# Kernel optimization log

Measured on AMD Instinct MI355X. Metric: run time of the kernel, lower is better.

The kernel has to match this reference:

```python
import jax, jax.numpy as jnp
import numpy as np

EPS = 1e-5
SLOPE = 0.2  # leakyrelu negative slope (gcn_lib default)
K = 9

def knn_idx(x, k):
    # x: (B, C, N) -> idx (B, N, k) of k nearest neighbors, self excluded
    B, C, N = x.shape
    xx = jnp.sum(x * x, axis=1)                       # (B, N)
    inner = jnp.einsum('bcn,bcm->bnm', x, x)          # (B, N, N)
    dist = xx[:, :, None] - 2.0 * inner + xx[:, None, :]
    dist = dist + jnp.eye(N, dtype=x.dtype) * 1e10    # mask self
    _, idx = jax.lax.top_k(-dist, k)                  # nearest = largest -dist
    return idx

def bn(h, g, b, axes):
    m = jnp.mean(h, axis=axes, keepdims=True)
    v = jnp.var(h, axis=axes, keepdims=True)
    sh = [1] * h.ndim; sh[1] = -1
    return (h - m) / jnp.sqrt(v + EPS) * g.reshape(sh) + b.reshape(sh)

def leaky(h):
    return jnp.where(h >= 0, h, SLOPE * h)

def edge_conv(x, idx, W, g, b):
    # x: (B, C, N); idx: (B, N, k); W: (O, 2C)
    B, C, N = x.shape
    k = idx.shape[-1]
    x_j = jax.vmap(lambda xb, ib: xb[:, ib])(x, idx)  # (B, C, N, k)
    x_i = jnp.broadcast_to(x[:, :, :, None], (B, C, N, k))
    edge = jnp.concatenate([x_i, x_j - x_i], axis=1)  # (B, 2C, N, k)
    h = jnp.einsum('oc,bcnk->bonk', W, edge)
    h = leaky(bn(h, g, b, (0, 2, 3)))
    return jnp.max(h, axis=-1)                        # (B, O, N)

def setup_inputs() -> dict:
    key = jax.random.key(0)
    ks = jax.random.split(key, 24)
    B, N = 8, 4096
    d = {}
    d['x'] = jax.random.normal(ks[0], (B, 3, N), dtype=jnp.float32)
    d['coords'] = jax.random.normal(ks[1], (B, 3, N), dtype=jnp.float32)
    def w(k_, o, i): return jax.random.normal(k_, (o, i), dtype=jnp.float32) * (2.0 / i) ** 0.5
    # edge conv layers (bias=False, batchnorm affine)
    d['w1'], d['g1'], d['b1'] = w(ks[2], 64, 6),    jnp.ones(64),  jnp.zeros(64)
    d['w2'], d['g2'], d['b2'] = w(ks[3], 64, 128),  jnp.ones(64),  jnp.zeros(64)
    d['w3'], d['g3'], d['b3'] = w(ks[4], 128, 128), jnp.ones(128), jnp.zeros(128)
    d['w4'], d['g4'], d['b4'] = w(ks[5], 256, 256), jnp.ones(256), jnp.zeros(256)
    # decoder fusion conv [512 -> 1024]
    d['wf'], d['bf'] = w(ks[6], 1024, 512), jnp.zeros(1024)
    d['gf'], d['betaf'] = jnp.ones(1024), jnp.zeros(1024)
    # classifier [2048 -> 512 -> 256 -> 40]
    d['wc1'], d['bc1'] = w(ks[7], 512, 2048), jnp.zeros(512)
    d['gc1'], d['betac1'] = jnp.ones(512), jnp.zeros(512)
    d['wc2'], d['bc2'] = w(ks[8], 256, 512), jnp.zeros(256)
    d['gc2'], d['betac2'] = jnp.ones(256), jnp.zeros(256)
    d['wc3'], d['bc3'] = w(ks[9], 40, 256), jnp.zeros(40)
    return d

def reference(x, coords, w1, g1, b1, w2, g2, b2, w3, g3, b3, w4, g4, b4,
              wf, bf, gf, betaf, wc1, bc1, gc1, betac1, wc2, bc2, gc2, betac2, wc3, bc3):
    out1 = edge_conv(x,    knn_idx(x, K),    w1, g1, b1)   # (B, 64, N)
    out2 = edge_conv(out1, knn_idx(out1, K), w2, g2, b2)   # (B, 64, N)
    out3 = edge_conv(out2, knn_idx(out2, K), w3, g3, b3)   # (B, 128, N)
    out4 = edge_conv(out3, knn_idx(out3, K), w4, g4, b4)   # (B, 256, N)
    feat = jnp.concatenate([out1, out2, out3, out4], axis=1)  # (B, 512, N)
    fusion = jnp.einsum('oc,bcn->bon', wf, feat) + bf[None, :, None]
    fusion = leaky(bn(fusion, gf, betaf, (0, 2)))           # (B, 1024, N)
    x1 = jnp.max(fusion, axis=-1)                           # adaptive max pool
    x2 = jnp.mean(fusion, axis=-1)                          # adaptive avg pool
    h = jnp.concatenate([x1, x2], axis=1)                   # (B, 2048)
    h = leaky(bn(h @ wc1.T + bc1, gc1, betac1, (0,)))       # dropout = identity (eval)
    h = leaky(bn(h @ wc2.T + bc2, gc2, betac2, (0,)))
    logits = h @ wc3.T + bc3                                # (B, 40)
    return logits
```

## Files before the change

kernel.cpp:

```cpp
#include <hip/hip_runtime.h>
#include <math.h>
#include <float.h>


#define LEAKY(y) ((y) >= 0.f ? (y) : 0.2f * (y))

using f32x16 = __attribute__((ext_vector_type(16))) float;
using bf16x8 = __attribute__((ext_vector_type(8))) __bf16;
using short8v = __attribute__((ext_vector_type(8))) short;

__device__ inline ushort f2bf(float x) {
  unsigned u = __float_as_uint(x);
  unsigned r = (u + 0x7fff + ((u >> 16) & 1)) >> 16;
  return (ushort)r;
}

template<int C>
__global__ void xx_kernel(const float* __restrict__ xin, long bstride, int N,
                          float* __restrict__ xxg) {
  int n = blockIdx.x * 256 + threadIdx.x;
  int b = blockIdx.y;
  if (n < N) {
    const float* xb = xin + (long)b * bstride;
    float s = 0.f;
    #pragma unroll
    for (int c = 0; c < C; ++c) { float t = xb[(long)c * N + n]; s += t * t; }
    xxg[(long)b * N + n] = s;
  }
}

template<int C, int KCc>
__global__ __launch_bounds__(256) void pack3_kernel(const float* __restrict__ xin, long bstride,
                                                    int N, const float* __restrict__ xxg,
                                                    ushort* __restrict__ packR,
                                                    ushort* __restrict__ packC,
                                                    float* __restrict__ xpm) {
  __shared__ float xt[C][32];
  const int tid = threadIdx.x;
  const int pb = blockIdx.x, b = blockIdx.y;
  for (int i = tid; i < C * 32; i += 256) {
    int c = i >> 5, j = i & 31;
    xt[c][j] = xin[(long)b * bstride + (long)c * N + pb * 32 + j];
  }
  __syncthreads();
  for (int i = tid; i < 32 * C; i += 256) {
    int pt = i / C, c = i % C;
    xpm[((long)b * N + pb * 32 + pt) * C + c] = xt[c][pt];
  }
  const int PB = N >> 5;
  for (int it = tid; it < KCc * 64; it += 256) {
    int kc = it >> 6, l = it & 63;
    int pt = l & 31;
    union { ushort u[8]; short8v v; } R, Cc;
    #pragma unroll
    for (int e = 0; e < 8; ++e) {
      int kp = kc * 16 + ((l >> 5) << 3) + e;
      ushort rv = 0, cv = 0;
      if (kp < 3 * C) {
        int s = kp / C, c = kp % C;
        float xv = xt[c][pt];
        ushort hi = f2bf(xv);
        float hif = __uint_as_float((unsigned)hi << 16);
        ushort mid = f2bf(xv - hif);
        rv = (s == 2) ? mid : hi;
        cv = (s == 1) ? mid : hi;
      } else if (kp == 3 * C) {
        float xxv = xxg[(long)b * N + pb * 32 + pt];
        cv = f2bf(xxv);
        rv = 0xBF00;
      } else if (kp == 3 * C + 1) {
        float xxv = xxg[(long)b * N + pb * 32 + pt];
        ushort hi = f2bf(xxv);
        float hif = __uint_as_float((unsigned)hi << 16);
        cv = f2bf(xxv - hif);
        rv = 0xBF00;
      }
      R.u[e] = rv; Cc.u[e] = cv;
    }
    long off = (((long)b * PB + pb) * KCc + kc) * 512 + l * 8;
    *reinterpret_cast<short8v*>(&packR[off]) = R.v;
    *reinterpret_cast<short8v*>(&packC[off]) = Cc.v;
  }
}

#define KNN_SCAN(SELF)                                            \
  _Pragma("unroll")                                               \
  for (int reg = 0; reg < 16; ++reg) {                            \
    int m_loc = (reg & 3) + 8 * (reg >> 2) + 4 * hf;              \
    float d = fmaf(-2.0f, acc[reg], xr);                          \
    d = fmaxf(d, 0.f);                                            \
    unsigned key = (__float_as_uint(d) & KEYMASK) |               \
                   (unsigned)((t << 5) | m_loc);                  \
    if (SELF && ((mb << 5) | m_loc) == n_glob) key = 0xFFFFFFFFu; \
    if (key < tk[9]) {                                            \
      unsigned kc = key;                                          \
      _Pragma("unroll")                                           \
      for (int s_ = 0; s_ < 10; ++s_) {                           \
        unsigned mn_ = min(kc, tk[s_]);                           \
        kc = max(kc, tk[s_]);                                     \
        tk[s_] = mn_;                                             \
      }                                                           \
    }                                                             \
  }

template<int KCc, int MINW, int Z>
__global__ __launch_bounds__(256, MINW) void knn_v5(const ushort* __restrict__ packR,
                                                    const ushort* __restrict__ packC,
                                                    const float* __restrict__ xxg,
                                                    int N, int* __restrict__ cand) {
  constexpr int SA_ELEMS = KCc * 512;
  constexpr int SA_BYTES = SA_ELEMS * 2;
  constexpr int POOL = (2 * SA_BYTES > 10240) ? 2 * SA_BYTES : 10240;
  __shared__ __align__(16) char smem[POOL];
  ushort* const sA0 = (ushort*)smem;
  ushort* const sA1 = (ushort*)(smem + SA_BYTES);

  const int tid = threadIdx.x;
  const int b = blockIdx.y, rowblk = blockIdx.x, z = blockIdx.z;
  const int w = tid >> 6, l = tid & 63;
  const int lane31 = l & 31, hf = l >> 5;
  const int PB = N >> 5;
  const int HALF = PB / Z;
  const unsigned IDXMASK = (unsigned)(HALF * 32 - 1);
  const unsigned KEYMASK = ~IDXMASK;
  const int myblk = rowblk * 4 + w;

  const ushort* rp = packR + (((long)b * PB + myblk) * (long)KCc) * 512 + l * 8;
  bf16x8 bfr[KCc];
  #pragma unroll
  for (int kc = 0; kc < KCc; ++kc)
    bfr[kc] = *reinterpret_cast<const bf16x8*>(rp + kc * 512);

  const ushort* srcb = packC + ((long)b * PB) * (long)SA_ELEMS;
  const int mb0 = z * HALF;

  {
    const ushort* src = srcb + (long)mb0 * SA_ELEMS;
    for (int i = tid * 8; i < SA_ELEMS; i += 2048)
      __builtin_amdgcn_global_load_lds(
          (const __attribute__((address_space(1))) void*)(src + i),
          (__attribute__((address_space(3))) void*)(sA0 + i), 16, 0, 0);
  }

  const int n_glob = rowblk * 128 + w * 32 + lane31;
  const float xr = xxg[(long)b * N + n_glob];

  unsigned tk[10];
  #pragma unroll
  for (int s = 0; s < 10; ++s) tk[s] = 0xFFFFFFFFu;

  __syncthreads();

  for (int t = 0; t < HALF; ++t) {
    const int mb = mb0 + t;
    const ushort* curA = (t & 1) ? sA1 : sA0;
    ushort* nxtA = (t & 1) ? sA0 : sA1;
    if (t + 1 < HALF) {
      const ushort* src = srcb + (long)(mb + 1) * SA_ELEMS;
      for (int i = tid * 8; i < SA_ELEMS; i += 2048)
        __builtin_amdgcn_global_load_lds(
            (const __attribute__((address_space(1))) void*)(src + i),
            (__attribute__((address_space(3))) void*)(nxtA + i), 16, 0, 0);
    }
    f32x16 acc = {};
    #pragma unroll
    for (int kc = 0; kc < KCc; ++kc) {
      bf16x8 af = *reinterpret_cast<const bf16x8*>(curA + kc * 512 + l * 8);
      acc = __builtin_amdgcn_mfma_f32_32x32x16_bf16(af, bfr[kc], acc, 0, 0, 0);
    }
    if (mb == myblk) {
      KNN_SCAN(true)
    } else {
      KNN_SCAN(false)
    }
    __syncthreads();
  }

  unsigned* mK = (unsigned*)smem;
  const int row = w * 32 + lane31;
  #pragma unroll
  for (int s = 0; s < 10; ++s)
    mK[row * 20 + hf * 10 + s] = tk[s];
  __syncthreads();
  if (tid < 128) {
    int p0 = 0, p1 = 0;
    const long ob = ((long)b * N + rowblk * 128 + tid) * (Z * 10) + z * 10;
    const int base_m = z * HALF * 32;
    for (int s = 0; s < 10; ++s) {
      unsigned k0 = mK[tid * 20 + p0];
      unsigned k1 = mK[tid * 20 + 10 + p1];
      bool t0 = k0 < k1;
      unsigned kk = t0 ? k0 : k1;
      cand[ob + s] = base_m + (int)(kk & IDXMASK);
      if (t0) ++p0; else ++p1;
    }
  }
}

template<int C, int P>
__global__ __launch_bounds__(320) void rerank_kernel(const float* __restrict__ xpm,
                                                     int N, const float* __restrict__ xxg,
                                                     const int* __restrict__ cand,
                                                     int* __restrict__ idx_out) {
  constexpr int ROWS = 320 / P;
  __shared__ float sq[ROWS][C];
  __shared__ float sd[ROWS][P + 1];
  __shared__ int   si[ROWS][P + 1];
  const int tid = threadIdx.x;
  const int b = blockIdx.y, n0 = blockIdx.x * ROWS;
  const float* xb = xpm + (long)b * N * C;
  for (int i = tid; i < ROWS * C; i += 320) {
    int r = i / C, c = i % C;
    sq[r][c] = xb[(long)(n0 + r) * C + c];
  }
  __syncthreads();
  const int r = tid / P, j = tid % P;
  const int n = n0 + r;
  const int m = cand[((long)b * N + n) * P + j];
  const float* cv = xb + (long)m * C;
  float dot = 0.f;
  if constexpr ((C & 3) == 0) {
    for (int c = 0; c < C; c += 4) {
      float4 v4 = *reinterpret_cast<const float4*>(cv + c);
      dot = fmaf(sq[r][c + 0], v4.x, dot);
      dot = fmaf(sq[r][c + 1], v4.y, dot);
      dot = fmaf(sq[r][c + 2], v4.z, dot);
      dot = fmaf(sq[r][c + 3], v4.w, dot);
    }
  } else {
    for (int c = 0; c < C; ++c) dot = fmaf(sq[r][c], cv[c], dot);
  }
  float d = (xxg[(long)b * N + n] - 2.0f * dot) + xxg[(long)b * N + m];
  if (m == n) d = 3.0e38f;
  sd[r][j] = d; si[r][j] = m;
  __syncthreads();
  int rank = 0;
  #pragma unroll
  for (int t = 0; t < P; ++t) {
    float dd = sd[r][t]; int ii = si[r][t];
    if (dd < d || (dd == d && ii < m)) rank++;
  }
  if (rank < 9) idx_out[((long)b * N + n) * 9 + rank] = m;
}

template<int C, int KCX>
__global__ __launch_bounds__(256) void pack6_x(const float* __restrict__ xin, long bstride,
                                               int N, ushort* __restrict__ packX) {
  __shared__ float xt[C][32];
  const int tid = threadIdx.x;
  const int pb = blockIdx.x, b = blockIdx.y;
  for (int i = tid; i < C * 32; i += 256) {
    int c = i >> 5, j = i & 31;
    xt[c][j] = xin[(long)b * bstride + (long)c * N + pb * 32 + j];
  }
  __syncthreads();
  const int PB = N >> 5;
  for (int it = tid; it < KCX * 64; it += 256) {
    int kc = it >> 6, l = it & 63;
    int pt = l & 31;
    union { ushort u[8]; short8v v; } P;
    #pragma unroll
    for (int e = 0; e < 8; ++e) {
      int kp = kc * 16 + ((l >> 5) << 3) + e;
      ushort val = 0;
      if (kp < 6 * C) {
        int s = kp / C, c = kp % C;
        float xv = xt[c][pt];
        ushort hi = f2bf(xv);
        float hif = __uint_as_float((unsigned)hi << 16);
        float r1 = xv - hif;
        ushort mid = f2bf(r1);
        float midf = __uint_as_float((unsigned)mid << 16);
        ushort lo = f2bf(r1 - midf);
        val = (s == 1 || s == 3) ? mid : ((s == 4) ? lo : hi);
      }
      P.u[e] = val;
    }
    long off = (((long)b * PB + pb) * KCX + kc) * 512 + l * 8;
    *reinterpret_cast<short8v*>(&packX[off]) = P.v;
  }
}

template<int C, int NOB, int KCW>
__global__ __launch_bounds__(256) void pack6_w(const float* __restrict__ W,
                                               ushort* __restrict__ packAw) {
  __shared__ float wt[32][C + 1];
  const int mo = blockIdx.x;
  const int mat = mo / NOB, ob = mo % NOB;
  const int tid = threadIdx.x;
  for (int i = tid; i < 32 * C; i += 256) {
    int o = i / C, c = i % C;
    float w1v = W[(long)(ob * 32 + o) * 2 * C + c];
    float w2v = W[(long)(ob * 32 + o) * 2 * C + C + c];
    wt[o][c] = mat ? w2v : (w1v - w2v);
  }
  __syncthreads();
  for (int it = tid; it < KCW * 64; it += 256) {
    int kc = it >> 6, l = it & 63;
    union { ushort u[8]; short8v v; } P;
    #pragma unroll
    for (int e = 0; e < 8; ++e) {
      int kp = kc * 16 + ((l >> 5) << 3) + e;
      ushort val = 0;
      if (kp < 6 * C) {
        int s = kp / C, c = kp % C;
        float xv = wt[l & 31][c];
        ushort hi = f2bf(xv);
        float hif = __uint_as_float((unsigned)hi << 16);
        float r1 = xv - hif;
        ushort mid = f2bf(r1);
        float midf = __uint_as_float((unsigned)mid << 16);
        ushort lo = f2bf(r1 - midf);
        val = (s == 2 || s == 3) ? mid : ((s == 5) ? lo : hi);
      }
      P.u[e] = val;
    }
    *reinterpret_cast<short8v*>(&packAw[((long)mo * KCW + kc) * 512 + l * 8]) = P.v;
  }
}

template<int KCW, int NOB>
__global__ __launch_bounds__(256) void edge_gemm6(const ushort* __restrict__ packX,
                                                  const ushort* __restrict__ packAw,
                                                  int N,
                                                  float* __restrict__ u,
                                                  float* __restrict__ v) {
  constexpr int NT = 2 * NOB;
  constexpr int TPW = NT / 4;
  constexpr int O = NOB * 32;
  const int nb = blockIdx.x, b = blockIdx.y;
  const int w = threadIdx.x >> 6, l = threadIdx.x & 63;
  const int lane31 = l & 31, hf = l >> 5;
  const ushort* xp = packX + ((long)(b * (N >> 5) + nb) * KCW) * 512 + l * 8;

  f32x16 acc[TPW] = {};
  const ushort* aptr[TPW];
  #pragma unroll
  for (int ti = 0; ti < TPW; ++ti) {
    int t = w + ti * 4;
    int mat = t & 1, ob = t >> 1;
    aptr[ti] = packAw + ((long)(mat * NOB + ob) * KCW) * 512 + l * 8;
  }

  for (int kc = 0; kc < KCW; ++kc) {
    bf16x8 bf = *reinterpret_cast<const bf16x8*>(xp + (long)kc * 512);
    #pragma unroll
    for (int ti = 0; ti < TPW; ++ti) {
      bf16x8 af = *reinterpret_cast<const bf16x8*>(aptr[ti] + (long)kc * 512);
      acc[ti] = __builtin_amdgcn_mfma_f32_32x32x16_bf16(af, bf, acc[ti], 0, 0, 0);
    }
  }

  #pragma unroll
  for (int ti = 0; ti < TPW; ++ti) {
    int t = w + ti * 4;
    int mat = t & 1, ob = t >> 1;
    float* dst = mat ? v : u;
    long rowbase = ((long)b * N + nb * 32 + lane31) * O + ob * 32;
    #pragma unroll
    for (int q = 0; q < 4; ++q) {
      float4 st = make_float4(acc[ti][4 * q + 0], acc[ti][4 * q + 1],
                              acc[ti][4 * q + 2], acc[ti][4 * q + 3]);
      *reinterpret_cast<float4*>(&dst[rowbase + 4 * hf + 8 * q]) = st;
    }
  }
}

__global__ __launch_bounds__(256) void edge_pass(const float* __restrict__ u,
                                                 const float* __restrict__ v,
                                                 const int* __restrict__ idx,
                                                 const float* __restrict__ g,
                                                 int O, int N,
                                                 float* __restrict__ hsel,
                                                 double* __restrict__ S1,
                                                 double* __restrict__ S2) {
  const int tid = threadIdx.x;
  const int n0 = blockIdx.x * 64, o0 = blockIdx.y * 64, b = blockIdx.z;
  __shared__ int sidx[64][9];
  __shared__ float4 redA[4][16];
  __shared__ float4 redB[4][16];
  for (int i = tid; i < 576; i += 256)
    ((int*)sidx)[i] = idx[((long)b * N + n0) * 9 + i];
  __syncthreads();
  const int nl = tid >> 4, oq = tid & 15;
  const long base = (long)b * N;
  const int ocol = o0 + 4 * oq;
  const float4 gv = *reinterpret_cast<const float4*>(&g[ocol]);
  float4 s1 = make_float4(0.f, 0.f, 0.f, 0.f);
  float4 s2 = make_float4(0.f, 0.f, 0.f, 0.f);
  for (int gg = 0; gg < 4; ++gg) {
    const int n = gg * 16 + nl;
    const float4 u4 = *reinterpret_cast<const float4*>(&u[(base + n0 + n) * O + ocol]);
    float4 mx = make_float4(-3.0e38f, -3.0e38f, -3.0e38f, -3.0e38f);
    float4 mn = make_float4(3.0e38f, 3.0e38f, 3.0e38f, 3.0e38f);
    #pragma unroll
    for (int k = 0; k < 9; ++k) {
      int m = sidx[n][k];
      const float4 v4 = *reinterpret_cast<const float4*>(&v[(base + m) * O + ocol]);
      float hx = u4.x + v4.x, hy = u4.y + v4.y, hz = u4.z + v4.z, hw = u4.w + v4.w;
      s1.x += hx; s1.y += hy; s1.z += hz; s1.w += hw;
      s2.x = fmaf(hx, hx, s2.x); s2.y = fmaf(hy, hy, s2.y);
      s2.z = fmaf(hz, hz, s2.z); s2.w = fmaf(hw, hw, s2.w);
      mx.x = fmaxf(mx.x, hx); mx.y = fmaxf(mx.y, hy); mx.z = fmaxf(mx.z, hz); mx.w = fmaxf(mx.w, hw);
      mn.x = fminf(mn.x, hx); mn.y = fminf(mn.y, hy); mn.z = fminf(mn.z, hz); mn.w = fminf(mn.w, hw);
    }
    float4 sel;
    sel.x = (gv.x >= 0.f) ? mx.x : mn.x;
    sel.y = (gv.y >= 0.f) ? mx.y : mn.y;
    sel.z = (gv.z >= 0.f) ? mx.z : mn.z;
    sel.w = (gv.w >= 0.f) ? mx.w : mn.w;
    *reinterpret_cast<float4*>(&hsel[(base + n0 + n) * O + ocol]) = sel;
  }
  s1.x += __shfl_xor(s1.x, 16); s1.y += __shfl_xor(s1.y, 16);
  s1.z += __shfl_xor(s1.z, 16); s1.w += __shfl_xor(s1.w, 16);
  s2.x += __shfl_xor(s2.x, 16); s2.y += __shfl_xor(s2.y, 16);
  s2.z += __shfl_xor(s2.z, 16); s2.w += __shfl_xor(s2.w, 16);
  s1.x += __shfl_xor(s1.x, 32); s1.y += __shfl_xor(s1.y, 32);
  s1.z += __shfl_xor(s1.z, 32); s1.w += __shfl_xor(s1.w, 32);
  s2.x += __shfl_xor(s2.x, 32); s2.y += __shfl_xor(s2.y, 32);
  s2.z += __shfl_xor(s2.w, 32) * 0.f + __shfl_xor(s2.z, 32); s2.w += __shfl_xor(s2.w, 32);
  if ((tid & 48) == 0) { redA[tid >> 6][oq] = s1; redB[tid >> 6][oq] = s2; }
  __syncthreads();
  if (tid < 16) {
    float4 a = redA[0][tid], bb = redB[0][tid];
    #pragma unroll
    for (int ww = 1; ww < 4; ++ww) {
      float4 t1 = redA[ww][tid], t2 = redB[ww][tid];
      a.x += t1.x; a.y += t1.y; a.z += t1.z; a.w += t1.w;
      bb.x += t2.x; bb.y += t2.y; bb.z += t2.z; bb.w += t2.w;
    }
    int o = o0 + 4 * tid;
    atomicAdd(&S1[o + 0], (double)a.x);  atomicAdd(&S1[o + 1], (double)a.y);
    atomicAdd(&S1[o + 2], (double)a.z);  atomicAdd(&S1[o + 3], (double)a.w);
    atomicAdd(&S2[o + 0], (double)bb.x); atomicAdd(&S2[o + 1], (double)bb.y);
    atomicAdd(&S2[o + 2], (double)bb.z); atomicAdd(&S2[o + 3], (double)bb.w);
  }
}

__global__ void finalize_scale(const double* __restrict__ S1, const double* __restrict__ S2,
                               const float* __restrict__ g, const float* __restrict__ beta,
                               double invM, int O, float* __restrict__ scale,
                               float* __restrict__ shift) {
  int o = blockIdx.x * 256 + threadIdx.x;
  if (o < O) {
    double mean = S1[o] * invM;
    double var = S2[o] * invM - mean * mean;
    double sc = (double)g[o] / sqrt(var + 1e-5);
    scale[o] = (float)sc;
    shift[o] = (float)((double)beta[o] - mean * sc);
  }
}

__global__ __launch_bounds__(256) void edge_out(const float* __restrict__ hsel,
                                                const float* __restrict__ scale,
                                                const float* __restrict__ shift,
                                                int O, int N,
                                                float* __restrict__ outp, long out_bstride) {
  const int tid = threadIdx.x;
  const int b = blockIdx.y, n0 = blockIdx.x * 64;
  __shared__ float yt[64][65];
  const int ol = tid & 63, nl = tid >> 6;
  const long base = (long)b * N;
  for (int oc = 0; oc < O; oc += 64) {
    float sc = scale[oc + ol], sh = shift[oc + ol];
    __syncthreads();
    for (int ng = 0; ng < 16; ++ng) {
      int n = ng * 4 + nl;
      float hv = hsel[(base + n0 + n) * O + oc + ol];
      float y = sc * hv + sh;
      yt[ol][n] = LEAKY(y);
    }
    __syncthreads();
    for (int rr = 0; rr < 16; ++rr) {
      int r = rr * 4 + nl;
      outp[(long)b * out_bstride + (long)(oc + r) * N + n0 + ol] = yt[r][ol];
    }
  }
}

__global__ __launch_bounds__(256) void pack3_wf(const float* __restrict__ wf,
                                                ushort* __restrict__ packW) {
  __shared__ float wt[32][129];
  const int po = blockIdx.x;
  const int tid = threadIdx.x;
  for (int c0 = 0; c0 < 512; c0 += 128) {
    __syncthreads();
    for (int i = tid; i < 32 * 128; i += 256) {
      int o = i >> 7, c = i & 127;
      wt[o][c] = wf[(long)(po * 32 + o) * 512 + c0 + c];
    }
    __syncthreads();
    #pragma unroll
    for (int s = 0; s < 3; ++s) {
      int kc0 = (s * 512 + c0) >> 4;
      for (int it = tid; it < 8 * 64; it += 256) {
        int kcl = it >> 6, l = it & 63;
        union { ushort u[8]; short8v v; } P;
        #pragma unroll
        for (int e = 0; e < 8; ++e) {
          int kp = (kc0 + kcl) * 16 + ((l >> 5) << 3) + e;
          int c = kp - s * 512 - c0;
          float xv = wt[l & 31][c];
          ushort hi = f2bf(xv);
          if (s == 1) {
            float hif = __uint_as_float((unsigned)hi << 16);
            P.u[e] = f2bf(xv - hif);
          } else P.u[e] = hi;
        }
        *reinterpret_cast<short8v*>(&packW[((long)po * 96 + kc0 + kcl) * 512 + l * 8]) = P.v;
      }
    }
  }
}

__global__ __launch_bounds__(256) void pack3_feat(const float* __restrict__ feat, int N,
                                                  ushort* __restrict__ packB) {
  __shared__ float xt[64][33];
  const int pb = blockIdx.x, b = blockIdx.y;
  const int tid = threadIdx.x;
  const int PB = N >> 5;
  for (int c0 = 0; c0 < 512; c0 += 64) {
    __syncthreads();
    for (int i = tid; i < 64 * 32; i += 256) {
      int c = i >> 5, j = i & 31;
      xt[c][j] = feat[((long)b * 512 + c0 + c) * N + pb * 32 + j];
    }
    __syncthreads();
    #pragma unroll
    for (int s = 0; s < 3; ++s) {
      int kc0 = (s * 512 + c0) >> 4;
      for (int it = tid; it < 4 * 64; it += 256) {
        int kcl = it >> 6, l = it & 63;
        union { ushort u[8]; short8v v; } P;
        #pragma unroll
        for (int e = 0; e < 8; ++e) {
          int kp = (kc0 + kcl) * 16 + ((l >> 5) << 3) + e;
          int c = kp - s * 512 - c0;
          float xv = xt[c][l & 31];
          ushort hi = f2bf(xv);
          if (s == 2) {
            float hif = __uint_as_float((unsigned)hi << 16);
            P.u[e] = f2bf(xv - hif);
          } else P.u[e] = hi;
        }
        *reinterpret_cast<short8v*>(
            &packB[(((long)b * PB + pb) * 96 + kc0 + kcl) * 512 + l * 8]) = P.v;
      }
    }
  }
}

#define FUS_EPI(ACC, Q)                                                          \
  _Pragma("unroll")                                                              \
  for (int reg = 0; reg < 16; ++reg) {                                           \
    int o = ((z * 16 + (Q) * 4 + w) << 5) + (reg & 3) + 8 * (reg >> 2) + 4 * hf; \
    float h = ACC[reg] + bfb[o];                                                 \
    hbf[((long)b * 1024 + o) * 4096 + (nt << 5) + lane31] = f2bf(h);             \
    float vsel = (gf[o] >= 0.f) ? h : -h;                                        \
    _Pragma("unroll")                                                            \
    for (int off = 1; off < 32; off <<= 1)                                       \
      vsel = fmaxf(vsel, __shfl_xor(vsel, off));                                 \
    if (lane31 == 0)                                                             \
      p3[(long)o * 1024 + b * 128 + nt] = vsel;                                  \
  }

__global__ __launch_bounds__(256) void fusion_gemm_store(const ushort* __restrict__ packW,
                                                         const ushort* __restrict__ packB,
                                                         const float* __restrict__ bfb,
                                                         const float* __restrict__ gf,
                                                         int N,
                                                         ushort* __restrict__ hbf,
                                                         float* __restrict__ p3) {
  __shared__ ushort sB[2][12 * 512];
  const int tid = threadIdx.x;
  const int nt = blockIdx.x, z = blockIdx.y, b = blockIdx.z;
  const int w = tid >> 6, l = tid & 63;
  const int lane31 = l & 31, hf = l >> 5;
  const int PB = N >> 5;
  const ushort* srcB = packB + (((long)b * PB + nt) * 96) * 512;

  for (int i = tid * 8; i < 12 * 512; i += 2048)
    __builtin_amdgcn_global_load_lds(
        (const __attribute__((address_space(1))) void*)(srcB + i),
        (__attribute__((address_space(3))) void*)(&sB[0][i]), 16, 0, 0);
  __syncthreads();

  f32x16 acc0 = {}, acc1 = {}, acc2 = {}, acc3 = {};
  const ushort* aw0 = packW + ((long)(z * 16 + 0 + w) * 96) * 512 + l * 8;
  const ushort* aw1 = packW + ((long)(z * 16 + 4 + w) * 96) * 512 + l * 8;
  const ushort* aw2 = packW + ((long)(z * 16 + 8 + w) * 96) * 512 + l * 8;
  const ushort* aw3 = packW + ((long)(z * 16 + 12 + w) * 96) * 512 + l * 8;

  int cur = 0;
  for (int ch = 0; ch < 8; ++ch) {
    if (ch + 1 < 8) {
      const ushort* src = srcB + (ch + 1) * 12 * 512;
      for (int i = tid * 8; i < 12 * 512; i += 2048)
        __builtin_amdgcn_global_load_lds(
            (const __attribute__((address_space(1))) void*)(src + i),
            (__attribute__((address_space(3))) void*)(&sB[cur ^ 1][i]), 16, 0, 0);
    }
    #pragma unroll
    for (int kcl = 0; kcl < 12; ++kcl) {
      const int kc = ch * 12 + kcl;
      bf16x8 bf = *reinterpret_cast<const bf16x8*>(&sB[cur][kcl * 512 + l * 8]);
      bf16x8 a0 = *reinterpret_cast<const bf16x8*>(aw0 + (long)kc * 512);
      acc0 = __builtin_amdgcn_mfma_f32_32x32x16_bf16(a0, bf, acc0, 0, 0, 0);
      bf16x8 a1 = *reinterpret_cast<const bf16x8*>(aw1 + (long)kc * 512);
      acc1 = __builtin_amdgcn_mfma_f32_32x32x16_bf16(a1, bf, acc1, 0, 0, 0);
      bf16x8 a2 = *reinterpret_cast<const bf16x8*>(aw2 + (long)kc * 512);
      acc2 = __builtin_amdgcn_mfma_f32_32x32x16_bf16(a2, bf, acc2, 0, 0, 0);
      bf16x8 a3 = *reinterpret_cast<const bf16x8*>(aw3 + (long)kc * 512);
      acc3 = __builtin_amdgcn_mfma_f32_32x32x16_bf16(a3, bf, acc3, 0, 0, 0);
    }
    __syncthreads();
    cur ^= 1;
  }

  FUS_EPI(acc0, 0)
  FUS_EPI(acc1, 1)
  FUS_EPI(acc2, 2)
  FUS_EPI(acc3, 3)
}

__global__ __launch_bounds__(256) void stats_bf16(const ushort* __restrict__ hbf,
                                                  float* __restrict__ ps1,
                                                  float* __restrict__ ps2) {
  int gw = (blockIdx.x * 256 + threadIdx.x) >> 6;
  int lane = threadIdx.x & 63;
  int b = gw >> 10, o = gw & 1023;
  const ushort* row = hbf + ((long)b * 1024 + o) * 4096;
  float s1 = 0.f, s2 = 0.f;
  for (int j = 0; j < 8; ++j) {
    union { ushort u[8]; short8v v; } hv;
    hv.v = *reinterpret_cast<const short8v*>(row + ((j << 6) + lane) * 8);
    #pragma unroll
    for (int e = 0; e < 8; ++e) {
      float h = __uint_as_float((unsigned)hv.u[e] << 16);
      s1 += h;
      s2 = fmaf(h, h, s2);
    }
  }
  #pragma unroll
  for (int off = 1; off < 64; off <<= 1) {
    s1 += __shfl_xor(s1, off);
    s2 += __shfl_xor(s2, off);
  }
  if (lane == 0) {
    ps1[(long)b * 1024 + o] = s1;
    ps2[(long)b * 1024 + o] = s2;
  }
}

__global__ void finalize_fusion2(const float* __restrict__ ps1, const float* __restrict__ ps2,
                                 const float* __restrict__ g, const float* __restrict__ beta,
                                 float* __restrict__ scale, float* __restrict__ shift) {
  int o = blockIdx.x * 256 + threadIdx.x;
  if (o < 1024) {
    double s1 = 0.0, s2 = 0.0;
    for (int b = 0; b < 8; ++b) {
      s1 += (double)ps1[(long)b * 1024 + o];
      s2 += (double)ps2[(long)b * 1024 + o];
    }
    double invM = 1.0 / 32768.0;
    double mean = s1 * invM;
    double var = s2 * invM - mean * mean;
    double sc = (double)g[o] / sqrt(var + 1e-5);
    scale[o] = (float)sc;
    shift[o] = (float)((double)beta[o] - mean * sc);
  }
}

__global__ __launch_bounds__(256) void pool_v3(const ushort* __restrict__ hbf,
                                               const float* __restrict__ p3,
                                               const float* __restrict__ scale,
                                               const float* __restrict__ shift,
                                               float* __restrict__ x1x2) {
  int gw = (blockIdx.x * 256 + threadIdx.x) >> 6;
  int lane = threadIdx.x & 63;
  int b = gw >> 10, o = gw & 1023;
  float sc = scale[o], sh = shift[o];

  long pb = (long)o * 1024 + b * 128;
  float red = fmaxf(p3[pb + lane], p3[pb + 64 + lane]);
  #pragma unroll
  for (int off = 1; off < 64; off <<= 1) red = fmaxf(red, __shfl_xor(red, off));
  float hm = (sc >= 0.f) ? red : -red;
  float x1 = LEAKY(fmaf(sc, hm, sh));

  const ushort* row = hbf + ((long)b * 1024 + o) * 4096;
  float sm = 0.f;
  for (int j = 0; j < 8; ++j) {
    union { ushort u[8]; short8v v; } hv;
    hv.v = *reinterpret_cast<const short8v*>(row + ((j << 6) + lane) * 8);
    #pragma unroll
    for (int e = 0; e < 8; ++e) {
      float h = __uint_as_float((unsigned)hv.u[e] << 16);
      float y = fmaf(sc, h, sh);
      sm += LEAKY(y);
    }
  }
  #pragma unroll
  for (int off = 1; off < 64; off <<= 1) sm += __shfl_xor(sm, off);

  if (lane == 0) {
    x1x2[(long)b * 2048 + o] = x1;
    x1x2[(long)b * 2048 + 1024 + o] = sm * (1.f / 4096.f);
  }
}

__global__ __launch_bounds__(256) void fc_kernel(const float* __restrict__ in, int Cin, int O,
                                                 const float* __restrict__ W,
                                                 const float* __restrict__ bias,
                                                 const float* __restrict__ g,
                                                 const float* __restrict__ beta,
                                                 float* __restrict__ outp, int do_bn) {
  const int tid = threadIdx.x;
  const int o = blockIdx.x * 32 + (tid >> 3);
  const int bb = tid & 7;
  const int oc = (o < O) ? o : (O - 1);
  const float* ir = in + (long)bb * Cin;
  const float* wr = W + (long)oc * Cin;
  float dot = 0.f;
  for (int c = 0; c < Cin; c += 4) {
    float4 a = *reinterpret_cast<const float4*>(&ir[c]);
    float4 w = *reinterpret_cast<const float4*>(&wr[c]);
    dot += a.x * w.x + a.y * w.y + a.z * w.z + a.w * w.w;
  }
  float h = dot + bias[oc];
  if (do_bn) {
    float s = h;
    s += __shfl_xor(s, 1, 8); s += __shfl_xor(s, 2, 8); s += __shfl_xor(s, 4, 8);
    float mean = s * 0.125f;
    float dv = (h - mean) * (h - mean);
    dv += __shfl_xor(dv, 1, 8); dv += __shfl_xor(dv, 2, 8); dv += __shfl_xor(dv, 4, 8);
    float var = dv * 0.125f;
    float y = (h - mean) * (float)(1.0 / sqrt((double)var + 1e-5)) * g[oc] + beta[oc];
    h = LEAKY(y);
  }
  if (o < O) outp[(long)bb * O + o] = h;
}

template<int Cin, int O>
static void edge_layer(const float* inp, long bstride, const float* W,
                       const float* g, const float* beta,
                       float* featOut, long out_bstride,
                       ushort* packX6, ushort* packAw, float* u, float* v,
                       const int* idx, float* hsel, double* S1, double* S2,
                       float* scale, float* shift, int N, int B,
                       hipStream_t stream) {
  constexpr int KCW = (6 * Cin + 15) / 16;
  constexpr int NOB = O / 32;
  pack6_x<Cin, KCW><<<dim3(N / 32, B), 256, 0, stream>>>(inp, bstride, N, packX6);
  pack6_w<Cin, NOB, KCW><<<2 * NOB, 256, 0, stream>>>(W, packAw);
  edge_gemm6<KCW, NOB><<<dim3(N / 32, B), 256, 0, stream>>>(packX6, packAw, N, u, v);
  hipMemsetAsync(S1, 0, O * 8, stream);
  hipMemsetAsync(S2, 0, O * 8, stream);
  edge_pass<<<dim3(N / 64, O / 64, B), 256, 0, stream>>>(u, v, idx, g, O, N, hsel, S1, S2);
  finalize_scale<<<(O + 255) / 256, 256, 0, stream>>>(S1, S2, g, beta,
                                                      1.0 / ((double)B * N * 9), O, scale, shift);
  edge_out<<<dim3(N / 64, B), 256, 0, stream>>>(hsel, scale, shift, O, N, featOut, out_bstride);
}

extern "C" void kernel_launch(void* const* d_in, const int* in_sizes, int n_in,
                              void* d_out, int out_size, void* d_ws, size_t ws_size,
                              hipStream_t stream) {
  const int B = 8, N = 4096;
  const float* x   = (const float*)d_in[0];
  const float* w1 = (const float*)d_in[2];  const float* g1 = (const float*)d_in[3];  const float* b1 = (const float*)d_in[4];
  const float* w2 = (const float*)d_in[5];  const float* g2 = (const float*)d_in[6];  const float* b2 = (const float*)d_in[7];
  const float* w3 = (const float*)d_in[8];  const float* g3 = (const float*)d_in[9];  const float* b3 = (const float*)d_in[10];
  const float* w4 = (const float*)d_in[11]; const float* g4 = (const float*)d_in[12]; const float* b4 = (const float*)d_in[13];
  const float* wf = (const float*)d_in[14]; const float* bfv = (const float*)d_in[15];
  const float* gf = (const float*)d_in[16]; const float* betaf = (const float*)d_in[17];
  const float* wc1 = (const float*)d_in[18]; const float* bc1 = (const float*)d_in[19];
  const float* gc1 = (const float*)d_in[20]; const float* betac1 = (const float*)d_in[21];
  const float* wc2 = (const float*)d_in[22]; const float* bc2 = (const float*)d_in[23];
  const float* gc2 = (const float*)d_in[24]; const float* betac2 = (const float*)d_in[25];
  const float* wc3 = (const float*)d_in[26]; const float* bc3 = (const float*)d_in[27];

  char* p = (char*)d_ws;
  auto alloc = [&](size_t bytes) -> char* {
    char* r = p;
    p += (bytes + 255) & ~(size_t)255;
    return r;
  };
  float* feat  = (float*)alloc((size_t)B * 512 * N * 4);
  int*   idx   = (int*)  alloc((size_t)B * N * 9 * 4);
  int*   cand  = (int*)  alloc((size_t)B * N * 64 * 4);
  float* xxg   = (float*)alloc((size_t)B * N * 4);
  float* u     = (float*)alloc((size_t)B * N * 256 * 4);
  float* v     = (float*)alloc((size_t)B * N * 256 * 4);
  float* hmax  = (float*)alloc((size_t)B * N * 256 * 4);
  float* hmin  = (float*)alloc((size_t)B * N * 256 * 4);
  ushort* packR = (ushort*)u;
  ushort* packC = (ushort*)hmax;
  float*  xpm   = hmin;
  ushort* packX6 = (ushort*)hmax;
  float*  hsel  = hmax;
  ushort* packB = (ushort*)u;
  ushort* hbf   = (ushort*)feat;
  float*  ps1   = hmin;
  float*  ps2   = hmin + 1048576;
  float*  ps3   = hmin + 2 * 1048576;
  ushort* packAw = (ushort*)alloc((size_t)2 * 8 * 48 * 512 * 2);
  ushort* packW = (ushort*)alloc((size_t)32 * 96 * 512 * 2);
  double* S1   = (double*)alloc(1024 * 8);
  double* S2   = (double*)alloc(1024 * 8);
  float* scale = (float*)alloc(1024 * 4);
  float* shift = (float*)alloc(1024 * 4);
  float* x1x2  = (float*)alloc((size_t)B * 2048 * 4);
  float* h1    = (float*)alloc((size_t)B * 512 * 4);
  float* h2    = (float*)alloc((size_t)B * 256 * 4);

  dim3 gpack(N / 32, B);
  dim3 gknn4(N / 128, B, 4);
  dim3 gknn2(N / 128, B, 2);
  dim3 grr40(N / 8, B);
  dim3 grr20(N / 16, B);
  dim3 gxx(N / 256, B);

  pack3_wf<<<32, 256, 0, stream>>>(wf, packW);

  xx_kernel<3><<<gxx, 256, 0, stream>>>(x, (long)3 * N, N, xxg);
  pack3_kernel<3, 1><<<gpack, 256, 0, stream>>>(x, (long)3 * N, N, xxg, packR, packC, xpm);
  knn_v5<1, 4, 4><<<gknn4, 256, 0, stream>>>(packR, packC, xxg, N, cand);
  rerank_kernel<3, 40><<<grr40, 320, 0, stream>>>(xpm, N, xxg, cand, idx);
  edge_layer<3, 64>(x, (long)3 * N, w1, g1, b1, feat, (long)512 * N,
                    packX6, packAw, u, v, idx, hsel, S1, S2, scale, shift, N, B, stream);

  xx_kernel<64><<<gxx, 256, 0, stream>>>(feat, (long)512 * N, N, xxg);
  pack3_kernel<64, 13><<<gpack, 256, 0, stream>>>(feat, (long)512 * N, N, xxg, packR, packC, xpm);
  knn_v5<13, 3, 4><<<gknn4, 256, 0, stream>>>(packR, packC, xxg, N, cand);
  rerank_kernel<64, 40><<<grr40, 320, 0, stream>>>(xpm, N, xxg, cand, idx);
  edge_layer<64, 64>(feat, (long)512 * N, w2, g2, b2, feat + (long)64 * N, (long)512 * N,
                     packX6, packAw, u, v, idx, hsel, S1, S2, scale, shift, N, B, stream);

  xx_kernel<64><<<gxx, 256, 0, stream>>>(feat + (long)64 * N, (long)512 * N, N, xxg);
  pack3_kernel<64, 13><<<gpack, 256, 0, stream>>>(feat + (long)64 * N, (long)512 * N, N, xxg,
                                                  packR, packC, xpm);
  knn_v5<13, 3, 4><<<gknn4, 256, 0, stream>>>(packR, packC, xxg, N, cand);
  rerank_kernel<64, 40><<<grr40, 320, 0, stream>>>(xpm, N, xxg, cand, idx);
  edge_layer<64, 128>(feat + (long)64 * N, (long)512 * N, w3, g3, b3,
                      feat + (long)128 * N, (long)512 * N,
                      packX6, packAw, u, v, idx, hsel, S1, S2, scale, shift, N, B, stream);

  xx_kernel<128><<<gxx, 256, 0, stream>>>(feat + (long)128 * N, (long)512 * N, N, xxg);
  pack3_kernel<128, 25><<<gpack, 256, 0, stream>>>(feat + (long)128 * N, (long)512 * N, N, xxg,
                                                   packR, packC, xpm);
  knn_v5<25, 3, 2><<<gknn2, 256, 0, stream>>>(packR, packC, xxg, N, cand);
  rerank_kernel<128, 20><<<grr20, 320, 0, stream>>>(xpm, N, xxg, cand, idx);
  edge_layer<128, 256>(feat + (long)128 * N, (long)512 * N, w4, g4, b4,
                       feat + (long)256 * N, (long)512 * N,
                       packX6, packAw, u, v, idx, hsel, S1, S2, scale, shift, N, B, stream);

  pack3_feat<<<dim3(N / 32, B), 256, 0, stream>>>(feat, N, packB);
  dim3 gfu(N / 32, 2, B);
  fusion_gemm_store<<<gfu, 256, 0, stream>>>(packW, packB, bfv, gf, N, hbf, ps3);
  stats_bf16<<<2048, 256, 0, stream>>>(hbf, ps1, ps2);
  finalize_fusion2<<<4, 256, 0, stream>>>(ps1, ps2, gf, betaf, scale, shift);
  pool_v3<<<2048, 256, 0, stream>>>(hbf, ps3, scale, shift, x1x2);

  fc_kernel<<<16, 256, 0, stream>>>(x1x2, 2048, 512, wc1, bc1, gc1, betac1, h1, 1);
  fc_kernel<<<8, 256, 0, stream>>>(h1, 512, 256, wc2, bc2, gc2, betac2, h2, 1);
  fc_kernel<<<2, 256, 0, stream>>>(h2, 256, 40, wc3, bc3, nullptr, nullptr, (float*)d_out, 0);
}
```

Measured before the change: 1.622 ms.

## Fuse per-layer packing kernels, replace double atomics with partials, split fusion GEMM finer

Merges the xx norm, kNN pack and edge-conv pack6_x into one pack_layer kernel that loads each tile once and computes squared norms in shared memory. Replaces the double-precision atomicAdd BN statistics (and their memsets) with per-block float partials, which a single-block finalize then sums. Halves the output channels per fusion_gemm block and doubles grid.z so more blocks run concurrently. It also reshuffles scratch buffer aliasing. The trade-off is a serial 512-term loop per channel in finalize_scale and more redundant B-tile loads in the fusion GEMM.

```diff
diff --git a/kernel.cpp b/kernel.cpp
--- a/kernel.cpp
+++ b/kernel.cpp
@@ -15,32 +15,27 @@
   return (ushort)r;
 }
 
-template<int C>
-__global__ void xx_kernel(const float* __restrict__ xin, long bstride, int N,
-                          float* __restrict__ xxg) {
-  int n = blockIdx.x * 256 + threadIdx.x;
-  int b = blockIdx.y;
-  if (n < N) {
-    const float* xb = xin + (long)b * bstride;
-    float s = 0.f;
-    #pragma unroll
-    for (int c = 0; c < C; ++c) { float t = xb[(long)c * N + n]; s += t * t; }
-    xxg[(long)b * N + n] = s;
-  }
-}
-
-template<int C, int KCc>
-__global__ __launch_bounds__(256) void pack3_kernel(const float* __restrict__ xin, long bstride,
-                                                    int N, const float* __restrict__ xxg,
-                                                    ushort* __restrict__ packR,
-                                                    ushort* __restrict__ packC,
-                                                    float* __restrict__ xpm) {
+template<int C, int KCc, int KCX>
+__global__ __launch_bounds__(256) void pack_layer(const float* __restrict__ xin, long bstride,
+                                                  int N, float* __restrict__ xxg,
+                                                  ushort* __restrict__ packR,
+                                                  ushort* __restrict__ packC,
+                                                  float* __restrict__ xpm,
+                                                  ushort* __restrict__ packX6) {
   __shared__ float xt[C][32];
+  __shared__ float sxx[32];
   const int tid = threadIdx.x;
   const int pb = blockIdx.x, b = blockIdx.y;
   for (int i = tid; i < C * 32; i += 256) {
     int c = i >> 5, j = i & 31;
     xt[c][j] = xin[(long)b * bstride + (long)c * N + pb * 32 + j];
+  }
+  __syncthreads();
+  if (tid < 32) {
+    float s = 0.f;
+    for (int c = 0; c < C; ++c) { float t = xt[c][tid]; s += t * t; }
+    sxx[tid] = s;
+    xxg[(long)b * N + pb * 32 + tid] = s;
   }
   __syncthreads();
   for (int i = tid; i < 32 * C; i += 256) {
@@ -65,11 +60,11 @@
         rv = (s == 2) ? mid : hi;
         cv = (s == 1) ? mid : hi;
       } else if (kp == 3 * C) {
-        float xxv = xxg[(long)b * N + pb * 32 + pt];
+        float xxv = sxx[pt];
         cv = f2bf(xxv);
         rv = 0xBF00;
       } else if (kp == 3 * C + 1) {
-        float xxv = xxg[(long)b * N + pb * 32 + pt];
+        float xxv = sxx[pt];
         ushort hi = f2bf(xxv);
         float hif = __uint_as_float((unsigned)hi << 16);
         cv = f2bf(xxv - hif);
@@ -80,6 +75,30 @@
     long off = (((long)b * PB + pb) * KCc + kc) * 512 + l * 8;
     *reinterpret_cast<short8v*>(&packR[off]) = R.v;
     *reinterpret_cast<short8v*>(&packC[off]) = Cc.v;
+  }
+  for (int it = tid; it < KCX * 64; it += 256) {
+    int kc = it >> 6, l = it & 63;
+    int pt = l & 31;
+    union { ushort u[8]; short8v v; } P;
+    #pragma unroll
+    for (int e = 0; e < 8; ++e) {
+      int kp = kc * 16 + ((l >> 5) << 3) + e;
+      ushort val = 0;
+      if (kp < 6 * C) {
+        int s = kp / C, c = kp % C;
+        float xv = xt[c][pt];
+        ushort hi = f2bf(xv);
+        float hif = __uint_as_float((unsigned)hi << 16);
+        float r1 = xv - hif;
+        ushort mid = f2bf(r1);
+        float midf = __uint_as_float((unsigned)mid << 16);
+        ushort lo = f2bf(r1 - midf);
+        val = (s == 1 || s == 3) ? mid : ((s == 4) ? lo : hi);
+      }
+      P.u[e] = val;
+    }
+    long off = (((long)b * PB + pb) * KCX + kc) * 512 + l * 8;
+    *reinterpret_cast<short8v*>(&packX6[off]) = P.v;
   }
 }
 
@@ -243,44 +262,6 @@
   if (rank < 9) idx_out[((long)b * N + n) * 9 + rank] = m;
 }
 
-template<int C, int KCX>
-__global__ __launch_bounds__(256) void pack6_x(const float* __restrict__ xin, long bstride,
-                                               int N, ushort* __restrict__ packX) {
-  __shared__ float xt[C][32];
-  const int tid = threadIdx.x;
-  const int pb = blockIdx.x, b = blockIdx.y;
-  for (int i = tid; i < C * 32; i += 256) {
-    int c = i >> 5, j = i & 31;
-    xt[c][j] = xin[(long)b * bstride + (long)c * N + pb * 32 + j];
-  }
-  __syncthreads();
-  const int PB = N >> 5;
-  for (int it = tid; it < KCX * 64; it += 256) {
-    int kc = it >> 6, l = it & 63;
-    int pt = l & 31;
-    union { ushort u[8]; short8v v; } P;
-    #pragma unroll
-    for (int e = 0; e < 8; ++e) {
-      int kp = kc * 16 + ((l >> 5) << 3) + e;
-      ushort val = 0;
-      if (kp < 6 * C) {
-        int s = kp / C, c = kp % C;
-        float xv = xt[c][pt];
-        ushort hi = f2bf(xv);
-        float hif = __uint_as_float((unsigned)hi << 16);
-        float r1 = xv - hif;
-        ushort mid = f2bf(r1);
-        float midf = __uint_as_float((unsigned)mid << 16);
-        ushort lo = f2bf(r1 - midf);
-        val = (s == 1 || s == 3) ? mid : ((s == 4) ? lo : hi);
-      }
-      P.u[e] = val;
-    }
-    long off = (((long)b * PB + pb) * KCX + kc) * 512 + l * 8;
-    *reinterpret_cast<short8v*>(&packX[off]) = P.v;
-  }
-}
-
 template<int C, int NOB, int KCW>
 __global__ __launch_bounds__(256) void pack6_w(const float* __restrict__ W,
                                                ushort* __restrict__ packAw) {
@@ -372,8 +353,8 @@
                                                  const float* __restrict__ g,
                                                  int O, int N,
                                                  float* __restrict__ hsel,
-                                                 double* __restrict__ S1,
-                                                 double* __restrict__ S2) {
+                                                 float* __restrict__ part1,
+                                                 float* __restrict__ part2) {
   const int tid = threadIdx.x;
   const int n0 = blockIdx.x * 64, o0 = blockIdx.y * 64, b = blockIdx.z;
   __shared__ int sidx[64][9];
@@ -418,7 +399,7 @@
   s1.x += __shfl_xor(s1.x, 32); s1.y += __shfl_xor(s1.y, 32);
   s1.z += __shfl_xor(s1.z, 32); s1.w += __shfl_xor(s1.w, 32);
   s2.x += __shfl_xor(s2.x, 32); s2.y += __shfl_xor(s2.y, 32);
-  s2.z += __shfl_xor(s2.w, 32) * 0.f + __shfl_xor(s2.z, 32); s2.w += __shfl_xor(s2.w, 32);
+  s2.z += __shfl_xor(s2.z, 32); s2.w += __shfl_xor(s2.w, 32);
   if ((tid & 48) == 0) { redA[tid >> 6][oq] = s1; redB[tid >> 6][oq] = s2; }
   __syncthreads();
   if (tid < 16) {
@@ -430,21 +411,27 @@
       bb.x += t2.x; bb.y += t2.y; bb.z += t2.z; bb.w += t2.w;
     }
     int o = o0 + 4 * tid;
-    atomicAdd(&S1[o + 0], (double)a.x);  atomicAdd(&S1[o + 1], (double)a.y);
-    atomicAdd(&S1[o + 2], (double)a.z);  atomicAdd(&S1[o + 3], (double)a.w);
-    atomicAdd(&S2[o + 0], (double)bb.x); atomicAdd(&S2[o + 1], (double)bb.y);
-    atomicAdd(&S2[o + 2], (double)bb.z); atomicAdd(&S2[o + 3], (double)bb.w);
-  }
-}
-
-__global__ void finalize_scale(const double* __restrict__ S1, const double* __restrict__ S2,
+    int part = b * gridDim.x + blockIdx.x;
+    part1[(long)(o + 0) * 512 + part] = a.x;  part2[(long)(o + 0) * 512 + part] = bb.x;
+    part1[(long)(o + 1) * 512 + part] = a.y;  part2[(long)(o + 1) * 512 + part] = bb.y;
+    part1[(long)(o + 2) * 512 + part] = a.z;  part2[(long)(o + 2) * 512 + part] = bb.z;
+    part1[(long)(o + 3) * 512 + part] = a.w;  part2[(long)(o + 3) * 512 + part] = bb.w;
+  }
+}
+
+__global__ void finalize_scale(const float* __restrict__ part1, const float* __restrict__ part2,
                                const float* __restrict__ g, const float* __restrict__ beta,
                                double invM, int O, float* __restrict__ scale,
                                float* __restrict__ shift) {
   int o = blockIdx.x * 256 + threadIdx.x;
   if (o < O) {
-    double mean = S1[o] * invM;
-    double var = S2[o] * invM - mean * mean;
+    double s1 = 0.0, s2 = 0.0;
+    for (int k = 0; k < 512; ++k) {
+      s1 += (double)part1[(long)o * 512 + k];
+      s2 += (double)part2[(long)o * 512 + k];
+    }
+    double mean = s1 * invM;
+    double var = s2 * invM - mean * mean;
     double sc = (double)g[o] / sqrt(var + 1e-5);
     scale[o] = (float)sc;
     shift[o] = (float)((double)beta[o] - mean * sc);
@@ -553,7 +540,7 @@
 #define FUS_EPI(ACC, Q)                                                          \
   _Pragma("unroll")                                                              \
   for (int reg = 0; reg < 16; ++reg) {                                           \
-    int o = ((z * 16 + (Q) * 4 + w) << 5) + (reg & 3) + 8 * (reg >> 2) + 4 * hf; \
+    int o = ((z * 8 + (Q) * 4 + w) << 5) + (reg & 3) + 8 * (reg >> 2) + 4 * hf;  \
     float h = ACC[reg] + bfb[o];                                                 \
     hbf[((long)b * 1024 + o) * 4096 + (nt << 5) + lane31] = f2bf(h);             \
     float vsel = (gf[o] >= 0.f) ? h : -h;                                        \
@@ -585,11 +572,9 @@
         (__attribute__((address_space(3))) void*)(&sB[0][i]), 16, 0, 0);
   __syncthreads();
 
-  f32x16 acc0 = {}, acc1 = {}, acc2 = {}, acc3 = {};
-  const ushort* aw0 = packW + ((long)(z * 16 + 0 + w) * 96) * 512 + l * 8;
-  const ushort* aw1 = packW + ((long)(z * 16 + 4 + w) * 96) * 512 + l * 8;
-  const ushort* aw2 = packW + ((long)(z * 16 + 8 + w) * 96) * 512 + l * 8;
-  const ushort* aw3 = packW + ((long)(z * 16 + 12 + w) * 96) * 512 + l * 8;
+  f32x16 acc0 = {}, acc1 = {};
+  const ushort* aw0 = packW + ((long)(z * 8 + 0 + w) * 96) * 512 + l * 8;
+  const ushort* aw1 = packW + ((long)(z * 8 + 4 + w) * 96) * 512 + l * 8;
 
   int cur = 0;
   for (int ch = 0; ch < 8; ++ch) {
@@ -608,10 +593,6 @@
       acc0 = __builtin_amdgcn_mfma_f32_32x32x16_bf16(a0, bf, acc0, 0, 0, 0);
       bf16x8 a1 = *reinterpret_cast<const bf16x8*>(aw1 + (long)kc * 512);
       acc1 = __builtin_amdgcn_mfma_f32_32x32x16_bf16(a1, bf, acc1, 0, 0, 0);
-      bf16x8 a2 = *reinterpret_cast<const bf16x8*>(aw2 + (long)kc * 512);
-      acc2 = __builtin_amdgcn_mfma_f32_32x32x16_bf16(a2, bf, acc2, 0, 0, 0);
-      bf16x8 a3 = *reinterpret_cast<const bf16x8*>(aw3 + (long)kc * 512);
-      acc3 = __builtin_amdgcn_mfma_f32_32x32x16_bf16(a3, bf, acc3, 0, 0, 0);
     }
     __syncthreads();
     cur ^= 1;
@@ -619,8 +600,6 @@
 
   FUS_EPI(acc0, 0)
   FUS_EPI(acc1, 1)
-  FUS_EPI(acc2, 2)
-  FUS_EPI(acc3, 3)
 }
 
 __global__ __launch_bounds__(256) void stats_bf16(const ushort* __restrict__ hbf,
@@ -742,23 +721,19 @@
 }
 
 template<int Cin, int O>
-static void edge_layer(const float* inp, long bstride, const float* W,
-                       const float* g, const float* beta,
+static void edge_layer(const float* W, const float* g, const float* beta,
                        float* featOut, long out_bstride,
-                       ushort* packX6, ushort* packAw, float* u, float* v,
-                       const int* idx, float* hsel, double* S1, double* S2,
+                       const ushort* packX6, ushort* packAw, float* u, float* v,
+                       const int* idx, float* hsel, float* part1, float* part2,
                        float* scale, float* shift, int N, int B,
                        hipStream_t stream) {
   constexpr int KCW = (6 * Cin + 15) / 16;
   constexpr int NOB = O / 32;
-  pack6_x<Cin, KCW><<<dim3(N / 32, B), 256, 0, stream>>>(inp, bstride, N, packX6);
   pack6_w<Cin, NOB, KCW><<<2 * NOB, 256, 0, stream>>>(W, packAw);
   edge_gemm6<KCW, NOB><<<dim3(N / 32, B), 256, 0, stream>>>(packX6, packAw, N, u, v);
-  hipMemsetAsync(S1, 0, O * 8, stream);
-  hipMemsetAsync(S2, 0, O * 8, stream);
-  edge_pass<<<dim3(N / 64, O / 64, B), 256, 0, stream>>>(u, v, idx, g, O, N, hsel, S1, S2);
-  finalize_scale<<<(O + 255) / 256, 256, 0, stream>>>(S1, S2, g, beta,
-                                                      1.0 / ((double)B * N * 9), O, scale, shift);
+  edge_pass<<<dim3(N / 64, O / 64, B), 256, 0, stream>>>(u, v, idx, g, O, N, hsel, part1, part2);
+  finalize_scale<<<1, 256, 0, stream>>>(part1, part2, g, beta,
+                                        1.0 / ((double)B * N * 9), O, scale, shift);
   edge_out<<<dim3(N / 64, B), 256, 0, stream>>>(hsel, scale, shift, O, N, featOut, out_bstride);
 }
 
@@ -794,10 +769,12 @@
   float* hmax  = (float*)alloc((size_t)B * N * 256 * 4);
   float* hmin  = (float*)alloc((size_t)B * N * 256 * 4);
   ushort* packR = (ushort*)u;
-  ushort* packC = (ushort*)hmax;
-  float*  xpm   = hmin;
+  ushort* packC = (ushort*)v;
   ushort* packX6 = (ushort*)hmax;
+  float*  xpm   = (float*)((char*)hmin + 16777216);
   float*  hsel  = hmax;
+  float*  part1 = hmin;
+  float*  part2 = hmin + 131072;
   ushort* packB = (ushort*)u;
   ushort* hbf   = (ushort*)feat;
   float*  ps1   = hmin;
@@ -805,8 +782,6 @@
   float*  ps3   = hmin + 2 * 1048576;
   ushort* packAw = (ushort*)alloc((size_t)2 * 8 * 48 * 512 * 2);
   ushort* packW = (ushort*)alloc((size_t)32 * 96 * 512 * 2);
-  double* S1   = (double*)alloc(1024 * 8);
-  double* S2   = (double*)alloc(1024 * 8);
   float* scale = (float*)alloc(1024 * 4);
   float* shift = (float*)alloc(1024 * 4);
   float* x1x2  = (float*)alloc((size_t)B * 2048 * 4);
@@ -818,44 +793,39 @@
   dim3 gknn2(N / 128, B, 2);
   dim3 grr40(N / 8, B);
   dim3 grr20(N / 16, B);
-  dim3 gxx(N / 256, B);
 
   pack3_wf<<<32, 256, 0, stream>>>(wf, packW);
 
-  xx_kernel<3><<<gxx, 256, 0, stream>>>(x, (long)3 * N, N, xxg);
-  pack3_kernel<3, 1><<<gpack, 256, 0, stream>>>(x, (long)3 * N, N, xxg, packR, packC, xpm);
+  pack_layer<3, 1, 2><<<gpack, 256, 0, stream>>>(x, (long)3 * N, N, xxg,
+                                                 packR, packC, xpm, packX6);
   knn_v5<1, 4, 4><<<gknn4, 256, 0, stream>>>(packR, packC, xxg, N, cand);
   rerank_kernel<3, 40><<<grr40, 320, 0, stream>>>(xpm, N, xxg, cand, idx);
-  edge_layer<3, 64>(x, (long)3 * N, w1, g1, b1, feat, (long)512 * N,
-                    packX6, packAw, u, v, idx, hsel, S1, S2, scale, shift, N, B, stream);
-
-  xx_kernel<64><<<gxx, 256, 0, stream>>>(feat, (long)512 * N, N, xxg);
-  pack3_kernel<64, 13><<<gpack, 256, 0, stream>>>(feat, (long)512 * N, N, xxg, packR, packC, xpm);
+  edge_layer<3, 64>(w1, g1, b1, feat, (long)512 * N, packX6, packAw, u, v, idx,
+                    hsel, part1, part2, scale, shift, N, B, stream);
+
+  pack_layer<64, 13, 24><<<gpack, 256, 0, stream>>>(feat, (long)512 * N, N, xxg,
+                                                    packR, packC, xpm, packX6);
   knn_v5<13, 3, 4><<<gknn4, 256, 0, stream>>>(packR, packC, xxg, N, cand);
   rerank_kernel<64, 40><<<grr40, 320, 0, stream>>>(xpm, N, xxg, cand, idx);
-  edge_layer<64, 64>(feat, (long)512 * N, w2, g2, b2, feat + (long)64 * N, (long)512 * N,
-                     packX6, packAw, u, v, idx, hsel, S1, S2, scale, shift, N, B, stream);
-
-  xx_kernel<64><<<gxx, 256, 0, stream>>>(feat + (long)64 * N, (long)512 * N, N, xxg);
-  pack3_kernel<64, 13><<<gpack, 256, 0, stream>>>(feat + (long)64 * N, (long)512 * N, N, xxg,
-                                                  packR, packC, xpm);
+  edge_layer<64, 64>(w2, g2, b2, feat + (long)64 * N, (long)512 * N, packX6, packAw,
+                     u, v, idx, hsel, part1, part2, scale, shift, N, B, stream);
+
+  pack_layer<64, 13, 24><<<gpack, 256, 0, stream>>>(feat + (long)64 * N, (long)512 * N, N, xxg,
+                                                    packR, packC, xpm, packX6);
   knn_v5<13, 3, 4><<<gknn4, 256, 0, stream>>>(packR, packC, xxg, N, cand);
   rerank_kernel<64, 40><<<grr40, 320, 0, stream>>>(xpm, N, xxg, cand, idx);
-  edge_layer<64, 128>(feat + (long)64 * N, (long)512 * N, w3, g3, b3,
-                      feat + (long)128 * N, (long)512 * N,
-                      packX6, packAw, u, v, idx, hsel, S1, S2, scale, shift, N, B, stream);
-
-  xx_kernel<128><<<gxx, 256, 0, stream>>>(feat + (long)128 * N, (long)512 * N, N, xxg);
-  pack3_kernel<128, 25><<<gpack, 256, 0, stream>>>(feat + (long)128 * N, (long)512 * N, N, xxg,
-                                                   packR, packC, xpm);
+  edge_layer<64, 128>(w3, g3, b3, feat + (long)128 * N, (long)512 * N, packX6, packAw,
+                      u, v, idx, hsel, part1, part2, scale, shift, N, B, stream);
+
+  pack_layer<128, 25, 48><<<gpack, 256, 0, stream>>>(feat + (long)128 * N, (long)512 * N, N, xxg,
+                                                     packR, packC, xpm, packX6);
   knn_v5<25, 3, 2><<<gknn2, 256, 0, stream>>>(packR, packC, xxg, N, cand);
   rerank_kernel<128, 20><<<grr20, 320, 0, stream>>>(xpm, N, xxg, cand, idx);
-  edge_layer<128, 256>(feat + (long)128 * N, (long)512 * N, w4, g4, b4,
-                       feat + (long)256 * N, (long)512 * N,
-                       packX6, packAw, u, v, idx, hsel, S1, S2, scale, shift, N, B, stream);
+  edge_layer<128, 256>(w4, g4, b4, feat + (long)256 * N, (long)512 * N, packX6, packAw,
+                       u, v, idx, hsel, part1, part2, scale, shift, N, B, stream);
 
   pack3_feat<<<dim3(N / 32, B), 256, 0, stream>>>(feat, N, packB);
-  dim3 gfu(N / 32, 2, B);
+  dim3 gfu(N / 32, 4, B);
   fusion_gemm_store<<<gfu, 256, 0, stream>>>(packW, packB, bfv, gf, N, hbf, ps3);
   stats_bf16<<<2048, 256, 0, stream>>>(hbf, ps1, ps2);
   finalize_fusion2<<<4, 256, 0, stream>>>(ps1, ps2, gf, betaf, scale, shift);
```

Result: faster. 1.501 ms (-7.4%).
